# Kernel optimization log

Measured on AMD Instinct MI355X. Metric: run time of the kernel, lower is better.

The kernel has to match this reference:

```python
import jax, jax.numpy as jnp
import numpy as np

T, IN_DIM, ISD, D, OUT = 512, 1024, 32, 256, 128
UP = D // ISD  # deconv kernel=stride=8, all-ones weight -> block upsample
DECAY, SPLIT, LOWER, FIRE, RESET = 0.9, 0.5, 0.1, 0.75, 0.0
EXC, INH, SCALE = 1.0, -0.5, 1.0
P_COARSE, P_FINE = 0.5, 0.8


def circ_avg(s, k, d):
    # circular 'same' conv with uniform 1/k^2 kernel (weight**0 then normalized)
    pad = d * (k - 1) // 2
    sp = jnp.pad(s, ((0, 0), (0, 0), (pad, pad), (pad, pad)), mode='wrap')
    w = jnp.full((1, 1, k, k), 1.0 / (k * k), dtype=s.dtype)
    return jax.lax.conv_general_dilated(sp, w, (1, 1), 'VALID', rhs_dilation=(d, d))


def setup_inputs() -> dict:
    key = jax.random.key(0)
    ks = jax.random.split(key, 6)
    X = jax.random.normal(ks[0], (T, IN_DIM), dtype=jnp.float32)
    perm = jax.random.permutation(ks[1], IN_DIM)
    We = jnp.eye(IN_DIM, dtype=jnp.float32)[perm]  # permuted identity embed weight
    mask_coarse = (jax.random.uniform(ks[2], (1, 1, ISD, ISD)) < P_COARSE).astype(jnp.float32)
    mask_fine = (jax.random.uniform(ks[3], (1, 1, D, D)) < P_FINE).astype(jnp.float32)
    W_out = jax.random.normal(ks[4], (OUT, 2, D, D), dtype=jnp.float32) * 0.01
    b_out = jax.random.normal(ks[5], (OUT,), dtype=jnp.float32) * 0.01
    return {"X": X, "We": We, "mask_coarse": mask_coarse, "mask_fine": mask_fine,
            "W_out": W_out, "b_out": b_out}


def _reservoir(X, We, mask_coarse, mask_fine):
    # CorticalInput: embed -> coarse mask -> ones-deconv (block upsample) -> tanh -> fine mask
    u = (X @ We.T).reshape(T, 1, ISD, ISD) * mask_coarse
    u = jnp.repeat(jnp.repeat(u, UP, axis=2), UP, axis=3)  # [T,1,D,D]
    u = SCALE * jnp.tanh(u) * mask_fine

    def step(carry, x_t):
        V, S = carry                     # [1,1,D,D]
        x_t = x_t[None]                  # [1,1,D,D]
        V = DECAY * V + SPLIT * x_t
        lat = EXC * circ_avg(S, 5, 1) + INH * circ_avg(S, 9, 2)
        V = jnp.where(V >= LOWER, V + (1.0 - SPLIT) * x_t + lat, V)
        V = jnp.minimum(V, 1.0)
        Sb = V > FIRE                    # dropout p=0 -> identity
        V = jnp.where(Sb, RESET, V)
        S = Sb.astype(V.dtype)
        return (V, S), jnp.stack([V[0, 0], S[0, 0]])  # [2,D,D]

    V0 = jnp.zeros((1, 1, D, D), dtype=jnp.float32)
    _, outs = jax.lax.scan(step, (V0, V0), u)  # [T,2,D,D]
    return outs


def reference(X, We, mask_coarse, mask_fine, W_out, b_out):
    outs = _reservoir(X, We, mask_coarse, mask_fine)
    # Conv2d(2, OUT, kernel=D) over [T,2,D,D] == dense readout, then squeeze
    return outs.reshape(T, -1) @ W_out.reshape(OUT, -1).T + b_out  # [T,OUT]
```

## Files before the change

### kernel.cpp

```cpp
#include <hip/hip_runtime.h>
#include <cstdint>


namespace {

constexpr int TT = 512;
constexpr int DD = 256;
constexpr int CELLS = DD * DD;
constexpr long KTOT = 2L * CELLS;
constexpr int TB = 128;
constexpr int NCH = TT / TB;
constexpr int KSLAB = 1024;
constexpr int NSLAB = 128;
constexpr int NW = 64;
constexpr long ACH = (long)TB * KTOT;

constexpr long OFF_PERM = 0;
constexpr long OFF_FLAG = 4096;
constexpr long OFF_VSAVE = OFF_FLAG + 8192;
constexpr long OFF_S = OFF_VSAVE + (long)CELLS * 4;
constexpr long OFF_A = OFF_S + 2L * CELLS * 4;
constexpr long OFF_P = OFF_A + 2L * ACH * 2;
constexpr long WS_REQUIRED = OFF_P + (long)NSLAB * TB * 128 * 4;

__device__ __forceinline__ int xcc_id() {
    int x;
    asm volatile("s_getreg_b32 %0, hwreg(HW_REG_XCC_ID, 0, 4)" : "=s"(x));
    return x;
}

__device__ __forceinline__ unsigned short f2bf(float x) {
    unsigned int u = __float_as_uint(x);
    u += 0x7FFFu + ((u >> 16) & 1u);
    return (unsigned short)(u >> 16);
}
__device__ __forceinline__ float bf2f(unsigned short b) {
    return __uint_as_float((unsigned int)b << 16);
}

__global__ __launch_bounds__(256) void perm_kernel(const float* __restrict__ We,
                                                   int* __restrict__ perm) {
    int idx = blockIdx.x * 256 + threadIdx.x;
    if (We[idx] > 0.5f) perm[idx >> 10] = idx & 1023;
}

__global__ void ctrl_init(int* __restrict__ flags, unsigned int* __restrict__ Spub,
                          int zero_spub) {
    int i = blockIdx.x * 256 + threadIdx.x;
    if (i == 0) { flags[1024] = 0; flags[1025] = 0; }
    if (zero_spub && i < (1 << 14)) {
        Spub[i] = 0u;
        Spub[i + (1 << 14)] = 0u;
    }
}

__global__ __launch_bounds__(256) void scan_gemm(
    const float* __restrict__ X,
    const int* __restrict__ perm,
    const float* __restrict__ mc,
    const float* __restrict__ mf,
    unsigned int* __restrict__ Spub,
    float* __restrict__ Vsave,
    unsigned short* __restrict__ Awr,
    int* __restrict__ flags,
    int t0,
    const unsigned short* __restrict__ Ard,
    const float* __restrict__ B,
    float* __restrict__ P,
    int gemm_on)
{
#pragma clang fp contract(off)
    __shared__ float4 C5L[4][64];
    __shared__ float4 C9L[4][64];
    __shared__ float As[16][68];
    __shared__ float Bs[16][132];
    __shared__ int sh_b;
    __shared__ int sh_g;

    const int tid = threadIdx.x;
    const int xcc = xcc_id();
    if (tid == 0) {
        int tk = -1, gk = -1;
        if (xcc == 0)
            tk = __hip_atomic_fetch_add(&flags[1024], 1, __ATOMIC_RELAXED,
                                        __HIP_MEMORY_SCOPE_AGENT);
        else if (gemm_on)
            gk = __hip_atomic_fetch_add(&flags[1025], 1, __ATOMIC_RELAXED,
                                        __HIP_MEMORY_SCOPE_AGENT);
        sh_b = tk;
        sh_g = gk;
    }
    __syncthreads();
    const int b = sh_b;
    const int gt = sh_g;

    if (b >= 0 && b < NW) {
        const int w = tid >> 6;
        const int l = tid & 63;
        const int row = b * 4 + w;
        const int cy = row >> 3;

        const int cc = cy * 32 + (l >> 1);
        const int pidx = perm[cc];
        const float mcv = mc[cc];

        constexpr int DYS10[10] = {-8, -6, -4, -2, -1, 1, 2, 4, 6, 8};
        int toff[10];
#pragma unroll
        for (int i = 0; i < 10; ++i)
            toff[i] = (((row + DYS10[i]) & 255) << 6) | l;

        float4 V;
        const float4 mfv = *(const float4*)&mf[row * DD + 4 * l];
        unsigned int own;
        if (t0 == 0) {
            V = make_float4(0.f, 0.f, 0.f, 0.f);
            own = 0u;
        } else {
            V = *(const float4*)&Vsave[row * DD + 4 * l];
            own = Spub[(((t0 + 1) & 1) << 14) + (row << 6) + l] & 0xFFFFu;
        }

        for (int t = t0; t < t0 + TB; ++t) {
            unsigned int tp[10];
            if (t > 0) {
                const unsigned int* base = Spub + (((t + 1) & 1) << 14);
                const unsigned int tag = (unsigned int)t;
                long g = 0;
                bool ok;
                do {
#pragma unroll
                    for (int i = 0; i < 10; ++i)
                        tp[i] = __hip_atomic_load(&base[toff[i]], __ATOMIC_RELAXED,
                                                  __HIP_MEMORY_SCOPE_AGENT);
                    bool mine = true;
#pragma unroll
                    for (int i = 0; i < 10; ++i) mine &= ((tp[i] >> 16) == tag);
                    ok = __all(mine);
                    if (++g > (1L << 18)) break;
                } while (!ok);
                if (!ok) break;
#pragma unroll
                for (int i = 0; i < 10; ++i) tp[i] &= 0xFFFFu;
            } else {
#pragma unroll
                for (int i = 0; i < 10; ++i) tp[i] = 0u;
            }

            const float um = tanhf(X[(long)t * 1024 + pidx] * mcv);

            const unsigned int c5i = tp[3] + tp[4] + own + tp[5] + tp[6];
            const unsigned int c9i = tp[0] + tp[1] + tp[2] + tp[3] + own
                                   + tp[6] + tp[7] + tp[8] + tp[9];
            float4 c5 = make_float4((float)(c5i & 0xFu), (float)((c5i >> 4) & 0xFu),
                                    (float)((c5i >> 8) & 0xFu), (float)((c5i >> 12) & 0xFu));
            float4 c9 = make_float4((float)(c9i & 0xFu), (float)((c9i >> 4) & 0xFu),
                                    (float)((c9i >> 8) & 0xFu), (float)((c9i >> 12) & 0xFu));

            C5L[w][l] = c5;
            C9L[w][l] = c9;
            __builtin_amdgcn_wave_barrier();
            float4 c5m  = C5L[w][(l + 63) & 63];
            float4 c5p  = C5L[w][(l + 1) & 63];
            float4 c9m2 = C5L[w][0].x == 0 && false ? c5 : C9L[w][(l + 62) & 63];
            c9m2 = C9L[w][(l + 62) & 63];
            float4 c9m1 = C9L[w][(l + 63) & 63];
            float4 c9p1 = C9L[w][(l + 1) & 63];
            float4 c9p2 = C9L[w][(l + 2) & 63];
            __builtin_amdgcn_wave_barrier();

            float e5[8] = {c5m.z, c5m.w, c5.x, c5.y, c5.z, c5.w, c5p.x, c5p.y};
            float e9[20] = {c9m2.x, c9m2.y, c9m2.z, c9m2.w,
                            c9m1.x, c9m1.y, c9m1.z, c9m1.w,
                            c9.x,   c9.y,   c9.z,   c9.w,
                            c9p1.x, c9p1.y, c9p1.z, c9p1.w,
                            c9p2.x, c9p2.y, c9p2.z, c9p2.w};
            float Vc[4]  = {V.x, V.y, V.z, V.w};
            float mfc[4] = {mfv.x, mfv.y, mfv.z, mfv.w};
            float Vn[4], Sn[4];
            unsigned int ipk = 0;
#pragma unroll
            for (int j = 0; j < 4; ++j) {
                float h5 = e5[j] + e5[j+1] + e5[j+2] + e5[j+3] + e5[j+4];
                float h9 = e9[j] + e9[j+2] + e9[j+4] + e9[j+6] + e9[j+8]
                         + e9[j+10] + e9[j+12] + e9[j+14] + e9[j+16];
                float avg5 = h5 * (1.0f/25.0f);
                float avg9 = h9 * (1.0f/81.0f);
                float lat = avg5 - 0.5f * avg9;
                float u = um * mfc[j];
                float V1 = 0.9f * Vc[j] + 0.5f * u;
                float V2 = (V1 >= 0.1f) ? ((V1 + 0.5f * u) + lat) : V1;
                V2 = fminf(V2, 1.0f);
                const bool sp = V2 > 0.75f;
                Vn[j] = sp ? 0.0f : V2;
                Sn[j] = sp ? 1.0f : 0.0f;
                if (sp) ipk |= 1u << (4 * j);
            }

            __hip_atomic_store(&Spub[((t & 1) << 14) + (row << 6) + l],
                               ipk | ((unsigned int)(t + 1) << 16),
                               __ATOMIC_RELAXED, __HIP_MEMORY_SCOPE_AGENT);
            own = ipk;

            unsigned short* Arow = Awr + (long)(t - t0) * KTOT;
            ushort4 uv, us;
            uv.x = f2bf(Vn[0]); uv.y = f2bf(Vn[1]); uv.z = f2bf(Vn[2]); uv.w = f2bf(Vn[3]);
            us.x = f2bf(Sn[0]); us.y = f2bf(Sn[1]); us.z = f2bf(Sn[2]); us.w = f2bf(Sn[3]);
            *(ushort4*)&Arow[row * DD + 4 * l] = uv;
            *(ushort4*)&Arow[CELLS + row * DD + 4 * l] = us;
            V = make_float4(Vn[0], Vn[1], Vn[2], Vn[3]);
        }

        *(float4*)&Vsave[row * DD + 4 * l] = V;
        return;
    }

    if (gt >= 0 && gt < 2 * NSLAB) {
        const int t0g = (gt & 1) * 64;
        const long k0 = (long)(gt >> 1) * KSLAB;
        const int tx = tid & 15;
        const int ty = tid >> 4;

        float acc[4][8];
#pragma unroll
        for (int i = 0; i < 4; ++i)
#pragma unroll
            for (int j = 0; j < 8; ++j) acc[i][j] = 0.0f;

        const int ar = tid >> 2, ac = (tid & 3) * 4;
        const int br = tid >> 1, bc = (tid & 1) * 8;

        for (int kc = 0; kc < KSLAB; kc += 16) {
            ushort4 av = *(const ushort4*)&Ard[(long)(t0g + ar) * KTOT + k0 + kc + ac];
            As[ac+0][ar] = bf2f(av.x); As[ac+1][ar] = bf2f(av.y);
            As[ac+2][ar] = bf2f(av.z); As[ac+3][ar] = bf2f(av.w);
            float4 bv0 = *(const float4*)&B[(long)br * KTOT + k0 + kc + bc];
            float4 bv1 = *(const float4*)&B[(long)br * KTOT + k0 + kc + bc + 4];
            Bs[bc+0][br] = bv0.x; Bs[bc+1][br] = bv0.y; Bs[bc+2][br] = bv0.z; Bs[bc+3][br] = bv0.w;
            Bs[bc+4][br] = bv1.x; Bs[bc+5][br] = bv1.y; Bs[bc+6][br] = bv1.z; Bs[bc+7][br] = bv1.w;
            __syncthreads();
#pragma unroll
            for (int kk = 0; kk < 16; ++kk) {
                float4 a4  = *(const float4*)&As[kk][ty*4];
                float4 b40 = *(const float4*)&Bs[kk][tx*8];
                float4 b41 = *(const float4*)&Bs[kk][tx*8+4];
                float a[4] = {a4.x, a4.y, a4.z, a4.w};
                float bb[8] = {b40.x, b40.y, b40.z, b40.w, b41.x, b41.y, b41.z, b41.w};
#pragma unroll
                for (int i = 0; i < 4; ++i)
#pragma unroll
                    for (int j = 0; j < 8; ++j) acc[i][j] += a[i] * bb[j];
            }
            __syncthreads();
        }
#pragma unroll
        for (int i = 0; i < 4; ++i)
#pragma unroll
            for (int j = 0; j < 8; ++j)
                P[((long)(gt >> 1) * TB + t0g + ty*4 + i) * 128 + tx*8 + j] = acc[i][j];
    }
}

__global__ __launch_bounds__(256) void gemm_partial(
    const unsigned short* __restrict__ A,
    const float* __restrict__ B,
    float* __restrict__ P)
{
    __shared__ float As[16][68];
    __shared__ float Bs[16][132];
    const int tid = threadIdx.x;
    const int t0 = blockIdx.x * 64;
    const long k0 = (long)blockIdx.y * KSLAB;
    const int tx = tid & 15;
    const int ty = tid >> 4;

    float acc[4][8];
#pragma unroll
    for (int i = 0; i < 4; ++i)
#pragma unroll
        for (int j = 0; j < 8; ++j) acc[i][j] = 0.0f;

    const int ar = tid >> 2, ac = (tid & 3) * 4;
    const int br = tid >> 1, bc = (tid & 1) * 8;

    for (int kc = 0; kc < KSLAB; kc += 16) {
        ushort4 av = *(const ushort4*)&A[(long)(t0 + ar) * KTOT + k0 + kc + ac];
        As[ac+0][ar] = bf2f(av.x); As[ac+1][ar] = bf2f(av.y);
        As[ac+2][ar] = bf2f(av.z); As[ac+3][ar] = bf2f(av.w);
        float4 bv0 = *(const float4*)&B[(long)br * KTOT + k0 + kc + bc];
        float4 bv1 = *(const float4*)&B[(long)br * KTOT + k0 + kc + bc + 4];
        Bs[bc+0][br] = bv0.x; Bs[bc+1][br] = bv0.y; Bs[bc+2][br] = bv0.z; Bs[bc+3][br] = bv0.w;
        Bs[bc+4][br] = bv1.x; Bs[bc+5][br] = bv1.y; Bs[bc+6][br] = bv1.z; Bs[bc+7][br] = bv1.w;
        __syncthreads();
#pragma unroll
        for (int kk = 0; kk < 16; ++kk) {
            float4 a4  = *(const float4*)&As[kk][ty*4];
            float4 b40 = *(const float4*)&Bs[kk][tx*8];
            float4 b41 = *(const float4*)&Bs[kk][tx*8+4];
            float a[4] = {a4.x, a4.y, a4.z, a4.w};
            float b[8] = {b40.x, b40.y, b40.z, b40.w, b41.x, b41.y, b41.z, b41.w};
#pragma unroll
            for (int i = 0; i < 4; ++i)
#pragma unroll
                for (int j = 0; j < 8; ++j) acc[i][j] += a[i] * b[j];
        }
        __syncthreads();
    }
#pragma unroll
    for (int i = 0; i < 4; ++i)
#pragma unroll
        for (int j = 0; j < 8; ++j)
            P[((long)blockIdx.y * TB + t0 + ty*4 + i) * 128 + tx*8 + j] = acc[i][j];
}

__global__ __launch_bounds__(256) void reduce_kernel(
    const float* __restrict__ P, const float* __restrict__ bias,
    float* __restrict__ out, int c)
{
    int tid = blockIdx.x * 256 + threadIdx.x;
    int o = tid & 127;
    float acc = 0.0f;
#pragma unroll 8
    for (int j = 0; j < NSLAB; ++j) acc += P[(long)j * (TB * 128) + tid];
    out[(long)c * (TB * 128) + tid] = acc + bias[o];
}

}

extern "C" void kernel_launch(void* const* d_in, const int* in_sizes, int n_in,
                              void* d_out, int out_size, void* d_ws, size_t ws_size,
                              hipStream_t stream)
{
    const float* X  = (const float*)d_in[0];
    const float* We = (const float*)d_in[1];
    const float* mc = (const float*)d_in[2];
    const float* mf = (const float*)d_in[3];
    const float* Wo = (const float*)d_in[4];
    const float* bo = (const float*)d_in[5];
    float* out = (float*)d_out;

    if (ws_size < (size_t)WS_REQUIRED) return;

    char* ws = (char*)d_ws;
    int*            perm   = (int*)(ws + OFF_PERM);
    int*            flags  = (int*)(ws + OFF_FLAG);
    float*          Vsave  = (float*)(ws + OFF_VSAVE);
    unsigned int*   Spub   = (unsigned int*)(ws + OFF_S);
    unsigned short* Achunk = (unsigned short*)(ws + OFF_A);
    float*          P      = (float*)(ws + OFF_P);

    perm_kernel<<<4096, 256, 0, stream>>>(We, perm);
    for (int c = 0; c < NCH; ++c) {
        ctrl_init<<<64, 256, 0, stream>>>(flags, Spub, c == 0 ? 1 : 0);
        scan_gemm<<<1024, 256, 0, stream>>>(
            X, perm, mc, mf, Spub, Vsave,
            Achunk + (long)(c & 1) * ACH,
            flags, c * TB,
            Achunk + (long)((c + 1) & 1) * ACH,
            Wo, P, c > 0 ? 1 : 0);
        if (c > 0)
            reduce_kernel<<<64, 256, 0, stream>>>(P, bo, out, c - 1);
    }
    gemm_partial<<<dim3(2, NSLAB), 256, 0, stream>>>(
        Achunk + (long)((NCH - 1) & 1) * ACH, Wo, P);
    reduce_kernel<<<64, 256, 0, stream>>>(P, bo, out, NCH - 1);
}
```

Measured before the change: 1.397 ms.

## Fuse readout reduction into scan kernel and drop per-chunk init launches

Removes the per-chunk ctrl_init and reduce_kernel launches. Their work moves into the persistent scan_gemm blocks on non-zero XCCs, using per-chunk counters and double-buffered partial sums so the reduction of chunk c-2 overlaps the scan. Also halves the number of K slabs by making each slab twice as long, which means fewer partials to reduce but half as many GEMM blocks. The final GEMM and the second-to-last reduction now share one launch.

```diff
diff --git a/kernel.cpp b/kernel.cpp
--- a/kernel.cpp
+++ b/kernel.cpp
@@ -10,10 +10,11 @@
 constexpr long KTOT = 2L * CELLS;
 constexpr int TB = 128;
 constexpr int NCH = TT / TB;
-constexpr int KSLAB = 1024;
-constexpr int NSLAB = 128;
+constexpr int KSLAB = 2048;
+constexpr int NSLAB = 64;
 constexpr int NW = 64;
 constexpr long ACH = (long)TB * KTOT;
+constexpr long PSZ = (long)NSLAB * TB * 128;
 
 constexpr long OFF_PERM = 0;
 constexpr long OFF_FLAG = 4096;
@@ -21,7 +22,7 @@
 constexpr long OFF_S = OFF_VSAVE + (long)CELLS * 4;
 constexpr long OFF_A = OFF_S + 2L * CELLS * 4;
 constexpr long OFF_P = OFF_A + 2L * ACH * 2;
-constexpr long WS_REQUIRED = OFF_P + (long)NSLAB * TB * 128 * 4;
+constexpr long WS_REQUIRED = OFF_P + 2L * PSZ * 4;
 
 __device__ __forceinline__ int xcc_id() {
     int x;
@@ -38,20 +39,14 @@
     return __uint_as_float((unsigned int)b << 16);
 }
 
-__global__ __launch_bounds__(256) void perm_kernel(const float* __restrict__ We,
-                                                   int* __restrict__ perm) {
+__global__ __launch_bounds__(256) void perm_init(
+    const float* __restrict__ We, int* __restrict__ perm,
+    int* __restrict__ flags, unsigned int* __restrict__ Spub)
+{
     int idx = blockIdx.x * 256 + threadIdx.x;
     if (We[idx] > 0.5f) perm[idx >> 10] = idx & 1023;
-}
-
-__global__ void ctrl_init(int* __restrict__ flags, unsigned int* __restrict__ Spub,
-                          int zero_spub) {
-    int i = blockIdx.x * 256 + threadIdx.x;
-    if (i == 0) { flags[1024] = 0; flags[1025] = 0; }
-    if (zero_spub && i < (1 << 14)) {
-        Spub[i] = 0u;
-        Spub[i + (1 << 14)] = 0u;
-    }
+    if (idx < 16) flags[1024 + idx] = 0;
+    if (idx < (1 << 15)) Spub[idx] = 0u;
 }
 
 __global__ __launch_bounds__(256) void scan_gemm(
@@ -63,11 +58,14 @@
     float* __restrict__ Vsave,
     unsigned short* __restrict__ Awr,
     int* __restrict__ flags,
-    int t0,
+    int t0, int c,
     const unsigned short* __restrict__ Ard,
     const float* __restrict__ B,
-    float* __restrict__ P,
-    int gemm_on)
+    float* __restrict__ Pwr,
+    const float* __restrict__ Prd,
+    const float* __restrict__ bias,
+    float* __restrict__ outPrev2,
+    int gemm_on, int reduce_on)
 {
 #pragma clang fp contract(off)
     __shared__ float4 C5L[4][64];
@@ -76,23 +74,31 @@
     __shared__ float Bs[16][132];
     __shared__ int sh_b;
     __shared__ int sh_g;
+    __shared__ int sh_r;
 
     const int tid = threadIdx.x;
     const int xcc = xcc_id();
     if (tid == 0) {
-        int tk = -1, gk = -1;
-        if (xcc == 0)
-            tk = __hip_atomic_fetch_add(&flags[1024], 1, __ATOMIC_RELAXED,
+        int tk = -1, gk = -1, rk = -1;
+        if (xcc == 0) {
+            tk = __hip_atomic_fetch_add(&flags[1024 + c], 1, __ATOMIC_RELAXED,
                                         __HIP_MEMORY_SCOPE_AGENT);
-        else if (gemm_on)
-            gk = __hip_atomic_fetch_add(&flags[1025], 1, __ATOMIC_RELAXED,
-                                        __HIP_MEMORY_SCOPE_AGENT);
+        } else {
+            if (gemm_on)
+                gk = __hip_atomic_fetch_add(&flags[1028 + c], 1, __ATOMIC_RELAXED,
+                                            __HIP_MEMORY_SCOPE_AGENT);
+            if ((gk < 0 || gk >= 2 * NSLAB) && reduce_on)
+                rk = __hip_atomic_fetch_add(&flags[1032 + c], 1, __ATOMIC_RELAXED,
+                                            __HIP_MEMORY_SCOPE_AGENT);
+        }
         sh_b = tk;
         sh_g = gk;
+        sh_r = rk;
     }
     __syncthreads();
     const int b = sh_b;
     const int gt = sh_g;
+    const int rt = sh_r;
 
     if (b >= 0 && b < NW) {
         const int w = tid >> 6;
@@ -162,8 +168,7 @@
             __builtin_amdgcn_wave_barrier();
             float4 c5m  = C5L[w][(l + 63) & 63];
             float4 c5p  = C5L[w][(l + 1) & 63];
-            float4 c9m2 = C5L[w][0].x == 0 && false ? c5 : C9L[w][(l + 62) & 63];
-            c9m2 = C9L[w][(l + 62) & 63];
+            float4 c9m2 = C9L[w][(l + 62) & 63];
             float4 c9m1 = C9L[w][(l + 63) & 63];
             float4 c9p1 = C9L[w][(l + 1) & 63];
             float4 c9p2 = C9L[w][(l + 2) & 63];
@@ -257,72 +262,97 @@
         for (int i = 0; i < 4; ++i)
 #pragma unroll
             for (int j = 0; j < 8; ++j)
-                P[((long)(gt >> 1) * TB + t0g + ty*4 + i) * 128 + tx*8 + j] = acc[i][j];
-    }
-}
-
-__global__ __launch_bounds__(256) void gemm_partial(
+                Pwr[((long)(gt >> 1) * TB + t0g + ty*4 + i) * 128 + tx*8 + j] = acc[i][j];
+        return;
+    }
+
+    if (rt >= 0 && rt < 64) {
+        int e = rt * 256 + tid;
+        int o = e & 127;
+        float acc = 0.0f;
+#pragma unroll 8
+        for (int j = 0; j < NSLAB; ++j) acc += Prd[(long)j * (TB * 128) + e];
+        outPrev2[e] = acc + bias[o];
+    }
+}
+
+__global__ __launch_bounds__(256) void gemm_tail(
     const unsigned short* __restrict__ A,
     const float* __restrict__ B,
-    float* __restrict__ P)
+    float* __restrict__ Pwr,
+    const float* __restrict__ Prd,
+    const float* __restrict__ bias,
+    float* __restrict__ outPrev)
 {
     __shared__ float As[16][68];
     __shared__ float Bs[16][132];
     const int tid = threadIdx.x;
-    const int t0 = blockIdx.x * 64;
-    const long k0 = (long)blockIdx.y * KSLAB;
-    const int tx = tid & 15;
-    const int ty = tid >> 4;
-
-    float acc[4][8];
-#pragma unroll
-    for (int i = 0; i < 4; ++i)
-#pragma unroll
-        for (int j = 0; j < 8; ++j) acc[i][j] = 0.0f;
-
-    const int ar = tid >> 2, ac = (tid & 3) * 4;
-    const int br = tid >> 1, bc = (tid & 1) * 8;
-
-    for (int kc = 0; kc < KSLAB; kc += 16) {
-        ushort4 av = *(const ushort4*)&A[(long)(t0 + ar) * KTOT + k0 + kc + ac];
-        As[ac+0][ar] = bf2f(av.x); As[ac+1][ar] = bf2f(av.y);
-        As[ac+2][ar] = bf2f(av.z); As[ac+3][ar] = bf2f(av.w);
-        float4 bv0 = *(const float4*)&B[(long)br * KTOT + k0 + kc + bc];
-        float4 bv1 = *(const float4*)&B[(long)br * KTOT + k0 + kc + bc + 4];
-        Bs[bc+0][br] = bv0.x; Bs[bc+1][br] = bv0.y; Bs[bc+2][br] = bv0.z; Bs[bc+3][br] = bv0.w;
-        Bs[bc+4][br] = bv1.x; Bs[bc+5][br] = bv1.y; Bs[bc+6][br] = bv1.z; Bs[bc+7][br] = bv1.w;
-        __syncthreads();
-#pragma unroll
-        for (int kk = 0; kk < 16; ++kk) {
-            float4 a4  = *(const float4*)&As[kk][ty*4];
-            float4 b40 = *(const float4*)&Bs[kk][tx*8];
-            float4 b41 = *(const float4*)&Bs[kk][tx*8+4];
-            float a[4] = {a4.x, a4.y, a4.z, a4.w};
-            float b[8] = {b40.x, b40.y, b40.z, b40.w, b41.x, b41.y, b41.z, b41.w};
-#pragma unroll
-            for (int i = 0; i < 4; ++i)
-#pragma unroll
-                for (int j = 0; j < 8; ++j) acc[i][j] += a[i] * b[j];
+    const int bid = blockIdx.x;
+
+    if (bid < 2 * NSLAB) {
+        const int t0g = (bid & 1) * 64;
+        const long k0 = (long)(bid >> 1) * KSLAB;
+        const int tx = tid & 15;
+        const int ty = tid >> 4;
+
+        float acc[4][8];
+#pragma unroll
+        for (int i = 0; i < 4; ++i)
+#pragma unroll
+            for (int j = 0; j < 8; ++j) acc[i][j] = 0.0f;
+
+        const int ar = tid >> 2, ac = (tid & 3) * 4;
+        const int br = tid >> 1, bc = (tid & 1) * 8;
+
+        for (int kc = 0; kc < KSLAB; kc += 16) {
+            ushort4 av = *(const ushort4*)&A[(long)(t0g + ar) * KTOT + k0 + kc + ac];
+            As[ac+0][ar] = bf2f(av.x); As[ac+1][ar] = bf2f(av.y);
+            As[ac+2][ar] = bf2f(av.z); As[ac+3][ar] = bf2f(av.w);
+            float4 bv0 = *(const float4*)&B[(long)br * KTOT + k0 + kc + bc];
+            float4 bv1 = *(const float4*)&B[(long)br * KTOT + k0 + kc + bc + 4];
+            Bs[bc+0][br] = bv0.x; Bs[bc+1][br] = bv0.y; Bs[bc+2][br] = bv0.z; Bs[bc+3][br] = bv0.w;
+            Bs[bc+4][br] = bv1.x; Bs[bc+5][br] = bv1.y; Bs[bc+6][br] = bv1.z; Bs[bc+7][br] = bv1.w;
+            __syncthreads();
+#pragma unroll
+            for (int kk = 0; kk < 16; ++kk) {
+                float4 a4  = *(const float4*)&As[kk][ty*4];
+                float4 b40 = *(const float4*)&Bs[kk][tx*8];
+                float4 b41 = *(const float4*)&Bs[kk][tx*8+4];
+                float a[4] = {a4.x, a4.y, a4.z, a4.w};
+                float bb[8] = {b40.x, b40.y, b40.z, b40.w, b41.x, b41.y, b41.z, b41.w};
+#pragma unroll
+                for (int i = 0; i < 4; ++i)
+#pragma unroll
+                    for (int j = 0; j < 8; ++j) acc[i][j] += a[i] * bb[j];
+            }
+            __syncthreads();
         }
-        __syncthreads();
-    }
-#pragma unroll
-    for (int i = 0; i < 4; ++i)
-#pragma unroll
-        for (int j = 0; j < 8; ++j)
-            P[((long)blockIdx.y * TB + t0 + ty*4 + i) * 128 + tx*8 + j] = acc[i][j];
+#pragma unroll
+        for (int i = 0; i < 4; ++i)
+#pragma unroll
+            for (int j = 0; j < 8; ++j)
+                Pwr[((long)(bid >> 1) * TB + t0g + ty*4 + i) * 128 + tx*8 + j] = acc[i][j];
+    } else {
+        int rt = bid - 2 * NSLAB;
+        int e = rt * 256 + tid;
+        int o = e & 127;
+        float acc = 0.0f;
+#pragma unroll 8
+        for (int j = 0; j < NSLAB; ++j) acc += Prd[(long)j * (TB * 128) + e];
+        outPrev[e] = acc + bias[o];
+    }
 }
 
 __global__ __launch_bounds__(256) void reduce_kernel(
     const float* __restrict__ P, const float* __restrict__ bias,
-    float* __restrict__ out, int c)
+    float* __restrict__ outP)
 {
-    int tid = blockIdx.x * 256 + threadIdx.x;
-    int o = tid & 127;
+    int e = blockIdx.x * 256 + threadIdx.x;
+    int o = e & 127;
     float acc = 0.0f;
 #pragma unroll 8
-    for (int j = 0; j < NSLAB; ++j) acc += P[(long)j * (TB * 128) + tid];
-    out[(long)c * (TB * 128) + tid] = acc + bias[o];
+    for (int j = 0; j < NSLAB; ++j) acc += P[(long)j * (TB * 128) + e];
+    outP[e] = acc + bias[o];
 }
 
 }
@@ -349,19 +379,22 @@
     unsigned short* Achunk = (unsigned short*)(ws + OFF_A);
     float*          P      = (float*)(ws + OFF_P);
 
-    perm_kernel<<<4096, 256, 0, stream>>>(We, perm);
+    perm_init<<<4096, 256, 0, stream>>>(We, perm, flags, Spub);
     for (int c = 0; c < NCH; ++c) {
-        ctrl_init<<<64, 256, 0, stream>>>(flags, Spub, c == 0 ? 1 : 0);
         scan_gemm<<<1024, 256, 0, stream>>>(
             X, perm, mc, mf, Spub, Vsave,
             Achunk + (long)(c & 1) * ACH,
-            flags, c * TB,
+            flags, c * TB, c,
             Achunk + (long)((c + 1) & 1) * ACH,
-            Wo, P, c > 0 ? 1 : 0);
-        if (c > 0)
-            reduce_kernel<<<64, 256, 0, stream>>>(P, bo, out, c - 1);
-    }
-    gemm_partial<<<dim3(2, NSLAB), 256, 0, stream>>>(
-        Achunk + (long)((NCH - 1) & 1) * ACH, Wo, P);
-    reduce_kernel<<<64, 256, 0, stream>>>(P, bo, out, NCH - 1);
-}
+            Wo,
+            P + (long)((c + 1) & 1) * PSZ,
+            P + (long)(c & 1) * PSZ,
+            bo,
+            out + (long)(c - 2) * TB * 128,
+            c > 0 ? 1 : 0, c > 1 ? 1 : 0);
+    }
+    gemm_tail<<<2 * NSLAB + 64, 256, 0, stream>>>(
+        Achunk + (long)((NCH - 1) & 1) * ACH, Wo,
+        P + PSZ, P, bo, out + 2L * TB * 128);
+    reduce_kernel<<<64, 256, 0, stream>>>(P + PSZ, bo, out + 3L * TB * 128);
+}
```

After: 1.797 ms. +28.6%, slower.
